# Kernel optimization log

Measured on AMD Instinct MI355X. Metric: run time of the kernel, lower is better.

Reference implementation:

```python
import jax, jax.numpy as jnp
import numpy as np

T, B, H, V, D = 128, 16, 8, 25, 64


def setup_inputs() -> dict:
    key = jax.random.key(0)
    k1, k2, k3 = jax.random.split(key, 3)
    q = jax.random.uniform(k1, (T, B, H, V, D), dtype=jnp.float32)
    kv = jax.random.uniform(k2, (T, B, H, V, D), dtype=jnp.float32)
    # decay factor in (0,1), per-head per-channel, as in the torch module
    decay = jax.random.uniform(k3, (1, 1, H, 1, D), dtype=jnp.float32)
    return {"q": q, "kv": kv, "decay": decay}


def reference(q, kv, decay):
    """Decay-based linear recurrent state-space scan (RetNet-style):
        S_t = decay * S_{t-1} + (1 - decay) * kv_t
        out_t = q_t * S_t
    q, kv: (T, B, H, V, D); decay: (1, 1, H, 1, D).
    """
    d = decay[0, 0]          # (H, 1, D), broadcasts against (B, H, V, D)
    one_minus_d = 1.0 - d

    def step(S, qkv_t):
        q_t, kv_t = qkv_t
        S = d * S + one_minus_d * kv_t
        return S, q_t * S

    S0 = jnp.zeros(q.shape[1:], dtype=q.dtype)  # (B, H, V, D)
    _, out = jax.lax.scan(step, S0, (q, kv))
    return out
```

## Files before the change

kernel.cpp:

```cpp
#include <hip/hip_runtime.h>


#define T_DIM 128
#define CH   204800
#define CH4  (CH / 4)
#define VD   (25 * 64)

__global__ __launch_bounds__(64) void sss_scan_v4(
    const float4* __restrict__ q,
    const float4* __restrict__ kv,
    const float*  __restrict__ decay,
    float4* __restrict__ out)
{
    const int i  = blockIdx.x * 64 + threadIdx.x;
    const int e0 = i * 4;
    const int dd = e0 & 63;
    const int h  = (e0 / VD) & 7;

    const float4 d   = *(const float4*)(decay + h * 64 + dd);
    const float4 omd = make_float4(1.0f - d.x, 1.0f - d.y, 1.0f - d.z, 1.0f - d.w);

    const float4* __restrict__ qp = q  + i;
    const float4* __restrict__ kp = kv + i;
    float4*       __restrict__ op = out + i;

    float4 S = make_float4(0.f, 0.f, 0.f, 0.f);

    float4 qa[4], ka[4], qb[4], kb[4];

    #pragma unroll
    for (int j = 0; j < 4; ++j) {
        ka[j] = kp[(size_t)j * CH4];
        qa[j] = qp[(size_t)j * CH4];
    }

    for (int g = 0; g < T_DIM / 4; ++g) {
        if (g + 1 < T_DIM / 4) {
            const int tb = (g + 1) * 4;
            #pragma unroll
            for (int j = 0; j < 4; ++j) {
                kb[j] = kp[(size_t)(tb + j) * CH4];
                qb[j] = qp[(size_t)(tb + j) * CH4];
            }
        }
        #pragma unroll
        for (int j = 0; j < 4; ++j) {
            S.x = fmaf(d.x, S.x, omd.x * ka[j].x);
            S.y = fmaf(d.y, S.y, omd.y * ka[j].y);
            S.z = fmaf(d.z, S.z, omd.z * ka[j].z);
            S.w = fmaf(d.w, S.w, omd.w * ka[j].w);
            float4 o;
            o.x = qa[j].x * S.x;
            o.y = qa[j].y * S.y;
            o.z = qa[j].z * S.z;
            o.w = qa[j].w * S.w;
            op[(size_t)(g * 4 + j) * CH4] = o;
        }
        #pragma unroll
        for (int j = 0; j < 4; ++j) { ka[j] = kb[j]; qa[j] = qb[j]; }
    }
}

extern "C" void kernel_launch(void* const* d_in, const int* in_sizes, int n_in,
                              void* d_out, int out_size, void* d_ws, size_t ws_size,
                              hipStream_t stream) {
    const float4* q     = (const float4*)d_in[0];
    const float4* kv    = (const float4*)d_in[1];
    const float*  decay = (const float*)d_in[2];
    float4* out = (float4*)d_out;

    const int threads = 64;
    const int blocks  = CH4 / threads;
    sss_scan_v4<<<blocks, threads, 0, stream>>>(q, kv, decay, out);
}
```

Baseline: 255.6 us.

## Split time scan into chunked two-pass scan for more parallelism

Replaces the single sequential time loop per channel with a two-pass chunked scan. Pass one computes each 16-step chunk's state contribution into workspace, and pass two combines prior chunk summaries using decay^16, then rescans its chunk to produce outputs. This multiplies the available threads to better saturate memory bandwidth, at the cost of reading kv twice plus small workspace traffic. Pass two also uses nontemporal loads and stores, and a simplified single-pass kernel remains as fallback when workspace is too small.

```diff
diff --git a/kernel.cpp b/kernel.cpp
--- a/kernel.cpp
+++ b/kernel.cpp
@@ -2,74 +2,139 @@
 
 
 #define T_DIM 128
-#define CH   204800
-#define CH4  (CH / 4)
-#define VD   (25 * 64)
+#define CH    204800
+#define CH4   (CH / 4)
+#define VD    (25 * 64)
+#define L_CHUNK 16
+#define N_CHUNK (T_DIM / L_CHUNK)
+#define BLK 256
+#define BLOCKS_PER_CHUNK (CH4 / BLK)
+
+typedef float f32x4 __attribute__((ext_vector_type(4)));
+
+static __device__ __forceinline__ f32x4 scan_step(f32x4 d, f32x4 omd, f32x4 S, f32x4 k) {
+    f32x4 r;
+    r[0] = fmaf(d[0], S[0], omd[0] * k[0]);
+    r[1] = fmaf(d[1], S[1], omd[1] * k[1]);
+    r[2] = fmaf(d[2], S[2], omd[2] * k[2]);
+    r[3] = fmaf(d[3], S[3], omd[3] * k[3]);
+    return r;
+}
+
+__global__ __launch_bounds__(BLK) void sss_pass1(
+    const f32x4* __restrict__ kv,
+    const float* __restrict__ decay,
+    f32x4* __restrict__ ws)
+{
+    const int b = blockIdx.x;
+    const int c = b / BLOCKS_PER_CHUNK;
+    const int i = (b % BLOCKS_PER_CHUNK) * BLK + threadIdx.x;
+    const int e0 = i * 4;
+    const int dd = e0 & 63;
+    const int h  = (e0 / VD) & 7;
+
+    const f32x4 d = *(const f32x4*)(decay + h * 64 + dd);
+    const f32x4 omd = 1.0f - d;
+
+    const f32x4* __restrict__ kp = kv + (size_t)c * L_CHUNK * CH4 + i;
+
+    f32x4 B = (f32x4)0.0f;
+    #pragma unroll
+    for (int j = 0; j < L_CHUNK; ++j) {
+        f32x4 k = kp[(size_t)j * CH4];
+        B = scan_step(d, omd, B, k);
+    }
+    ws[(size_t)c * CH4 + i] = B;
+}
+
+__global__ __launch_bounds__(BLK) void sss_pass2(
+    const f32x4* __restrict__ q,
+    const f32x4* __restrict__ kv,
+    const float* __restrict__ decay,
+    const f32x4* __restrict__ ws,
+    f32x4* __restrict__ out)
+{
+    const int b = blockIdx.x;
+    const int c = b / BLOCKS_PER_CHUNK;
+    const int i = (b % BLOCKS_PER_CHUNK) * BLK + threadIdx.x;
+    const int e0 = i * 4;
+    const int dd = e0 & 63;
+    const int h  = (e0 / VD) & 7;
+
+    const f32x4 d = *(const f32x4*)(decay + h * 64 + dd);
+    const f32x4 omd = 1.0f - d;
+
+    f32x4 A = d;
+    A = A * A;
+    A = A * A;
+    A = A * A;
+    A = A * A;
+
+    f32x4 S = (f32x4)0.0f;
+    for (int cp = 0; cp < c; ++cp) {
+        f32x4 B = ws[(size_t)cp * CH4 + i];
+        S[0] = fmaf(A[0], S[0], B[0]);
+        S[1] = fmaf(A[1], S[1], B[1]);
+        S[2] = fmaf(A[2], S[2], B[2]);
+        S[3] = fmaf(A[3], S[3], B[3]);
+    }
+
+    const size_t base = (size_t)c * L_CHUNK * CH4 + i;
+    const f32x4* __restrict__ kp = kv + base;
+    const f32x4* __restrict__ qp = q + base;
+    f32x4* __restrict__ op = out + base;
+
+    #pragma unroll
+    for (int j = 0; j < L_CHUNK; ++j) {
+        f32x4 k  = kp[(size_t)j * CH4];
+        f32x4 qq = __builtin_nontemporal_load(qp + (size_t)j * CH4);
+        S = scan_step(d, omd, S, k);
+        f32x4 o = qq * S;
+        __builtin_nontemporal_store(o, op + (size_t)j * CH4);
+    }
+}
 
 __global__ __launch_bounds__(64) void sss_scan_v4(
-    const float4* __restrict__ q,
-    const float4* __restrict__ kv,
-    const float*  __restrict__ decay,
-    float4* __restrict__ out)
+    const f32x4* __restrict__ q,
+    const f32x4* __restrict__ kv,
+    const float* __restrict__ decay,
+    f32x4* __restrict__ out)
 {
     const int i  = blockIdx.x * 64 + threadIdx.x;
     const int e0 = i * 4;
     const int dd = e0 & 63;
     const int h  = (e0 / VD) & 7;
 
-    const float4 d   = *(const float4*)(decay + h * 64 + dd);
-    const float4 omd = make_float4(1.0f - d.x, 1.0f - d.y, 1.0f - d.z, 1.0f - d.w);
+    const f32x4 d = *(const f32x4*)(decay + h * 64 + dd);
+    const f32x4 omd = 1.0f - d;
 
-    const float4* __restrict__ qp = q  + i;
-    const float4* __restrict__ kp = kv + i;
-    float4*       __restrict__ op = out + i;
+    const f32x4* __restrict__ qp = q  + i;
+    const f32x4* __restrict__ kp = kv + i;
+    f32x4*       __restrict__ op = out + i;
 
-    float4 S = make_float4(0.f, 0.f, 0.f, 0.f);
-
-    float4 qa[4], ka[4], qb[4], kb[4];
-
-    #pragma unroll
-    for (int j = 0; j < 4; ++j) {
-        ka[j] = kp[(size_t)j * CH4];
-        qa[j] = qp[(size_t)j * CH4];
-    }
-
-    for (int g = 0; g < T_DIM / 4; ++g) {
-        if (g + 1 < T_DIM / 4) {
-            const int tb = (g + 1) * 4;
-            #pragma unroll
-            for (int j = 0; j < 4; ++j) {
-                kb[j] = kp[(size_t)(tb + j) * CH4];
-                qb[j] = qp[(size_t)(tb + j) * CH4];
-            }
-        }
-        #pragma unroll
-        for (int j = 0; j < 4; ++j) {
-            S.x = fmaf(d.x, S.x, omd.x * ka[j].x);
-            S.y = fmaf(d.y, S.y, omd.y * ka[j].y);
-            S.z = fmaf(d.z, S.z, omd.z * ka[j].z);
-            S.w = fmaf(d.w, S.w, omd.w * ka[j].w);
-            float4 o;
-            o.x = qa[j].x * S.x;
-            o.y = qa[j].y * S.y;
-            o.z = qa[j].z * S.z;
-            o.w = qa[j].w * S.w;
-            op[(size_t)(g * 4 + j) * CH4] = o;
-        }
-        #pragma unroll
-        for (int j = 0; j < 4; ++j) { ka[j] = kb[j]; qa[j] = qb[j]; }
+    f32x4 S = (f32x4)0.0f;
+    for (int t = 0; t < T_DIM; ++t) {
+        f32x4 k  = kp[(size_t)t * CH4];
+        f32x4 qq = qp[(size_t)t * CH4];
+        S = scan_step(d, omd, S, k);
+        op[(size_t)t * CH4] = qq * S;
     }
 }
 
 extern "C" void kernel_launch(void* const* d_in, const int* in_sizes, int n_in,
                               void* d_out, int out_size, void* d_ws, size_t ws_size,
                               hipStream_t stream) {
-    const float4* q     = (const float4*)d_in[0];
-    const float4* kv    = (const float4*)d_in[1];
-    const float*  decay = (const float*)d_in[2];
-    float4* out = (float4*)d_out;
+    const f32x4* q     = (const f32x4*)d_in[0];
+    const f32x4* kv    = (const f32x4*)d_in[1];
+    const float* decay = (const float*)d_in[2];
+    f32x4* out = (f32x4*)d_out;
 
-    const int threads = 64;
-    const int blocks  = CH4 / threads;
-    sss_scan_v4<<<blocks, threads, 0, stream>>>(q, kv, decay, out);
+    const size_t ws_need = (size_t)N_CHUNK * CH4 * sizeof(f32x4);
+    if (d_ws != nullptr && ws_size >= ws_need) {
+        f32x4* ws = (f32x4*)d_ws;
+        sss_pass1<<<N_CHUNK * BLOCKS_PER_CHUNK, BLK, 0, stream>>>(kv, decay, ws);
+        sss_pass2<<<N_CHUNK * BLOCKS_PER_CHUNK, BLK, 0, stream>>>(q, kv, decay, ws, out);
+    } else {
+        sss_scan_v4<<<CH4 / 64, 64, 0, stream>>>(q, kv, decay, out);
+    }
 }
```

New measurement: 259.6 us. About the same (+1.6%).

## Use rolling 8-deep prefetch ring with full unroll and nontemporal stores

Applied to the files above, without the earlier changes.

Replaces the double-buffered 4-step groups with a fully unrolled ring buffer of 8 timesteps. Each step refills its slot with data 8 steps ahead, so more loads stay in flight per thread. Output stores are marked nontemporal to keep streaming writes from polluting cache, and scheduling barriers pin the load and compute order. The cost is higher register use and a larger unrolled body, and the barriers may stop the compiler from scheduling better on its own.

```diff
diff --git a/kernel.cpp b/kernel.cpp
--- a/kernel.cpp
+++ b/kernel.cpp
@@ -2,74 +2,71 @@
 
 
 #define T_DIM 128
-#define CH   204800
-#define CH4  (CH / 4)
-#define VD   (25 * 64)
+#define CH    204800
+#define CH4   (CH / 4)
+#define VD    (25 * 64)
+#define DEPTH 8
 
-__global__ __launch_bounds__(64) void sss_scan_v4(
-    const float4* __restrict__ q,
-    const float4* __restrict__ kv,
-    const float*  __restrict__ decay,
-    float4* __restrict__ out)
+typedef float f32x4 __attribute__((ext_vector_type(4)));
+
+__global__ __launch_bounds__(64) void sss_scan_v6(
+    const f32x4* __restrict__ q,
+    const f32x4* __restrict__ kv,
+    const float* __restrict__ decay,
+    f32x4* __restrict__ out)
 {
     const int i  = blockIdx.x * 64 + threadIdx.x;
     const int e0 = i * 4;
     const int dd = e0 & 63;
     const int h  = (e0 / VD) & 7;
 
-    const float4 d   = *(const float4*)(decay + h * 64 + dd);
-    const float4 omd = make_float4(1.0f - d.x, 1.0f - d.y, 1.0f - d.z, 1.0f - d.w);
+    const f32x4 d   = *(const f32x4*)(decay + h * 64 + dd);
+    const f32x4 omd = 1.0f - d;
 
-    const float4* __restrict__ qp = q  + i;
-    const float4* __restrict__ kp = kv + i;
-    float4*       __restrict__ op = out + i;
+    const f32x4* __restrict__ qp = q  + i;
+    const f32x4* __restrict__ kp = kv + i;
+    f32x4*       __restrict__ op = out + i;
 
-    float4 S = make_float4(0.f, 0.f, 0.f, 0.f);
+    f32x4 S = (f32x4)0.0f;
 
-    float4 qa[4], ka[4], qb[4], kb[4];
+    f32x4 kbuf[DEPTH], qbuf[DEPTH];
 
     #pragma unroll
-    for (int j = 0; j < 4; ++j) {
-        ka[j] = kp[(size_t)j * CH4];
-        qa[j] = qp[(size_t)j * CH4];
+    for (int t = 0; t < DEPTH; ++t) {
+        kbuf[t] = kp[(size_t)t * CH4];
+        qbuf[t] = qp[(size_t)t * CH4];
     }
+    __builtin_amdgcn_sched_barrier(0);
 
-    for (int g = 0; g < T_DIM / 4; ++g) {
-        if (g + 1 < T_DIM / 4) {
-            const int tb = (g + 1) * 4;
-            #pragma unroll
-            for (int j = 0; j < 4; ++j) {
-                kb[j] = kp[(size_t)(tb + j) * CH4];
-                qb[j] = qp[(size_t)(tb + j) * CH4];
-            }
+    #pragma unroll
+    for (int t = 0; t < T_DIM; ++t) {
+        const int j = t & (DEPTH - 1);
+
+        S[0] = fmaf(d[0], S[0], omd[0] * kbuf[j][0]);
+        S[1] = fmaf(d[1], S[1], omd[1] * kbuf[j][1]);
+        S[2] = fmaf(d[2], S[2], omd[2] * kbuf[j][2]);
+        S[3] = fmaf(d[3], S[3], omd[3] * kbuf[j][3]);
+
+        f32x4 o = qbuf[j] * S;
+        __builtin_nontemporal_store(o, op + (size_t)t * CH4);
+
+        if (t + DEPTH < T_DIM) {
+            kbuf[j] = kp[(size_t)(t + DEPTH) * CH4];
+            qbuf[j] = qp[(size_t)(t + DEPTH) * CH4];
         }
-        #pragma unroll
-        for (int j = 0; j < 4; ++j) {
-            S.x = fmaf(d.x, S.x, omd.x * ka[j].x);
-            S.y = fmaf(d.y, S.y, omd.y * ka[j].y);
-            S.z = fmaf(d.z, S.z, omd.z * ka[j].z);
-            S.w = fmaf(d.w, S.w, omd.w * ka[j].w);
-            float4 o;
-            o.x = qa[j].x * S.x;
-            o.y = qa[j].y * S.y;
-            o.z = qa[j].z * S.z;
-            o.w = qa[j].w * S.w;
-            op[(size_t)(g * 4 + j) * CH4] = o;
-        }
-        #pragma unroll
-        for (int j = 0; j < 4; ++j) { ka[j] = kb[j]; qa[j] = qb[j]; }
+        __builtin_amdgcn_sched_barrier(0);
     }
 }
 
 extern "C" void kernel_launch(void* const* d_in, const int* in_sizes, int n_in,
                               void* d_out, int out_size, void* d_ws, size_t ws_size,
                               hipStream_t stream) {
-    const float4* q     = (const float4*)d_in[0];
-    const float4* kv    = (const float4*)d_in[1];
-    const float*  decay = (const float*)d_in[2];
-    float4* out = (float4*)d_out;
+    const f32x4* q     = (const f32x4*)d_in[0];
+    const f32x4* kv    = (const f32x4*)d_in[1];
+    const float* decay = (const float*)d_in[2];
+    f32x4* out = (f32x4*)d_out;
 
     const int threads = 64;
     const int blocks  = CH4 / threads;
-    sss_scan_v4<<<blocks, threads, 0, stream>>>(q, kv, decay, out);
+    sss_scan_v6<<<blocks, threads, 0, stream>>>(q, kv, decay, out);
 }
```

Result: no change. 259.9 us (+1.7%).
